# Kernel optimization log

Hardware: AMD Instinct MI355X
Metric: run time of the kernel (lower is better)

The kernel has to match this reference:

```python
import jax, jax.numpy as jnp
import numpy as np

B, S, D, H = 4, 2048, 1024, 16
DK = D // H

def setup_inputs() -> dict:
    key = jax.random.key(0)
    ks = jax.random.split(key, 11)
    s = 1.0 / np.sqrt(D)
    return {
        "query": jax.random.normal(ks[0], (B, S, D), jnp.float32),
        "key": jax.random.normal(ks[1], (B, S, D), jnp.float32),
        "value": jax.random.normal(ks[2], (B, S, D), jnp.float32),
        "Wq_w": jax.random.normal(ks[3], (D, D), jnp.float32) * s,
        "Wq_b": jnp.zeros((D,), jnp.float32),
        "Wk_w": jax.random.normal(ks[4], (D, D), jnp.float32) * s,
        "Wk_b": jnp.zeros((D,), jnp.float32),
        "Wv_w": jax.random.normal(ks[5], (D, D), jnp.float32) * s,
        "Wv_b": jnp.zeros((D,), jnp.float32),
        "Wo_w": jax.random.normal(ks[6], (D, D), jnp.float32) * s,
        "Wo_b": jnp.zeros((D,), jnp.float32),
    }

def reference(query, key, value, Wq_w, Wq_b, Wk_w, Wk_b, Wv_w, Wv_b, Wo_w, Wo_b):
    b, s, d = query.shape
    # Linear projections (torch Linear: x @ W.T + b)
    q = query @ Wq_w.T + Wq_b
    k = key @ Wk_w.T + Wk_b
    v = value @ Wv_w.T + Wv_b
    # split heads -> [B, H, S, DK]
    q = q.reshape(b, s, H, DK).transpose(0, 2, 1, 3)
    k = k.reshape(b, s, H, DK).transpose(0, 2, 1, 3)
    v = v.reshape(b, s, H, DK).transpose(0, 2, 1, 3)
    # scaled dot-product attention
    scores = jnp.einsum("bhqd,bhkd->bhqk", q, k) / jnp.sqrt(jnp.asarray(DK, q.dtype))
    attn = jax.nn.softmax(scores, axis=-1)
    z = jnp.einsum("bhqk,bhkd->bhqd", attn, v)
    # merge heads and output projection
    z = z.transpose(0, 2, 1, 3).reshape(b, s, H * DK)
    return z @ Wo_w.T + Wo_b
```

## Files before the change

kernel.cpp:

```cpp
#include <hip/hip_runtime.h>
#include <stdint.h>

typedef unsigned short u16;
typedef __bf16 bf16x8 __attribute__((ext_vector_type(8)));
typedef float f32x4 __attribute__((ext_vector_type(4)));

#define B_   4
#define S_   2048
#define D_   1024
#define H_   16
#define DK_  64
#define MTOK (B_*S_)
#define LOG2E 1.4426950408889634f

static __device__ __forceinline__ float exp2_fast(float x){
  return __builtin_amdgcn_exp2f(x);
}

static __device__ __forceinline__ void gload_lds16(const void* g, void* l){
  __builtin_amdgcn_global_load_lds(
      (const __attribute__((address_space(1))) unsigned int*)g,
      (__attribute__((address_space(3))) unsigned int*)l, 16, 0, 0);
}

union bf8pack { __bf16 h[8]; uint4 u; };

__global__ void cvt4(const float* __restrict__ s0, const float* __restrict__ s1,
                     const float* __restrict__ s2, const float* __restrict__ s3,
                     u16* __restrict__ out, int n8){
  const float* s = blockIdx.y==0 ? s0 : blockIdx.y==1 ? s1 : blockIdx.y==2 ? s2 : s3;
  u16* o = out + (size_t)blockIdx.y * ((size_t)n8 * 8);
  int i = blockIdx.x * blockDim.x + threadIdx.x;
  int stride = gridDim.x * blockDim.x;
  for (; i < n8; i += stride){
    float4 v0 = reinterpret_cast<const float4*>(s)[i*2];
    float4 v1 = reinterpret_cast<const float4*>(s)[i*2+1];
    bf8pack p;
    p.h[0]=(__bf16)v0.x; p.h[1]=(__bf16)v0.y; p.h[2]=(__bf16)v0.z; p.h[3]=(__bf16)v0.w;
    p.h[4]=(__bf16)v1.x; p.h[5]=(__bf16)v1.y; p.h[6]=(__bf16)v1.z; p.h[7]=(__bf16)v1.w;
    reinterpret_cast<uint4*>(o)[i] = p.u;
  }
}

__global__ __launch_bounds__(256) void gemm_qkv(
    const float* __restrict__ q_in, const float* __restrict__ k_in, const float* __restrict__ v_in,
    const u16* __restrict__ wq, const u16* __restrict__ wk, const u16* __restrict__ wv,
    const float* __restrict__ bq, const float* __restrict__ bk, const float* __restrict__ bv,
    u16* __restrict__ Qb, u16* __restrict__ Kb, u16* __restrict__ VtG){
  const int z = blockIdx.z;
  const float* Ap   = z==0 ? q_in : z==1 ? k_in : v_in;
  const u16*   Bw   = z==0 ? wq : z==1 ? wk : wv;
  const float* bias = z==0 ? bq : z==1 ? bk : bv;
  const float scale = z==0 ? 0.125f*LOG2E : 1.0f;
  u16* Cb = z==0 ? Qb : z==1 ? Kb : VtG;

  __shared__ u16 As[2][128][32];
  __shared__ u16 Bs[2][128][32];
  const int tid  = threadIdx.x;
  const int lane = tid & 63;
  const int wid  = tid >> 6;
  const int wr = wid >> 1, wc = wid & 1;
  const int r15 = lane & 15, q4 = lane >> 4;
  const int id = blockIdx.x;
  const int bm = (id & 7) + ((id >> 6) << 3);
  const int bn = (id >> 3) & 7;
  const int K = D_, N = D_;
  const int NT = K / 32;

  const int r = tid >> 2, c = (tid & 3) << 3;
  const float* Ar0 = Ap + (size_t)(bm*128 + r)*K + c;
  const float* Ar1 = Ap + (size_t)(bm*128 + r + 64)*K + c;
  const u16*  Br0 = Bw + (size_t)(bn*128 + r)*K + c;
  const u16*  Br1 = Bw + (size_t)(bn*128 + r + 64)*K + c;

  f32x4 acc[4][4] = {};

  {
    float4 v00 = *reinterpret_cast<const float4*>(Ar0);
    float4 v01 = *reinterpret_cast<const float4*>(Ar0 + 4);
    float4 v10 = *reinterpret_cast<const float4*>(Ar1);
    float4 v11 = *reinterpret_cast<const float4*>(Ar1 + 4);
    bf8pack p0, p1;
    p0.h[0]=(__bf16)v00.x; p0.h[1]=(__bf16)v00.y; p0.h[2]=(__bf16)v00.z; p0.h[3]=(__bf16)v00.w;
    p0.h[4]=(__bf16)v01.x; p0.h[5]=(__bf16)v01.y; p0.h[6]=(__bf16)v01.z; p0.h[7]=(__bf16)v01.w;
    p1.h[0]=(__bf16)v10.x; p1.h[1]=(__bf16)v10.y; p1.h[2]=(__bf16)v10.z; p1.h[3]=(__bf16)v10.w;
    p1.h[4]=(__bf16)v11.x; p1.h[5]=(__bf16)v11.y; p1.h[6]=(__bf16)v11.z; p1.h[7]=(__bf16)v11.w;
    *reinterpret_cast<uint4*>(&As[0][r][c])    = p0.u;
    *reinterpret_cast<uint4*>(&As[0][r+64][c]) = p1.u;
    gload_lds16(Br0, &Bs[0][r][c]);
    gload_lds16(Br1, &Bs[0][r+64][c]);
  }
  __syncthreads();

  for (int t = 0; t < NT; ++t){
    const int cur = t & 1;
    float4 v00, v01, v10, v11;
    const bool pf = (t + 1 < NT);
    if (pf){
      const float* p0 = Ar0 + (t+1)*32;
      const float* p1 = Ar1 + (t+1)*32;
      v00 = *reinterpret_cast<const float4*>(p0);
      v01 = *reinterpret_cast<const float4*>(p0 + 4);
      v10 = *reinterpret_cast<const float4*>(p1);
      v11 = *reinterpret_cast<const float4*>(p1 + 4);
      gload_lds16(Br0 + (t+1)*32, &Bs[cur^1][r][c]);
      gload_lds16(Br1 + (t+1)*32, &Bs[cur^1][r+64][c]);
    }

    bf16x8 af[4], bfr[4];
    #pragma unroll
    for (int mf = 0; mf < 4; ++mf)
      af[mf] = *reinterpret_cast<const bf16x8*>(&As[cur][wr*64 + mf*16 + r15][q4*8]);
    #pragma unroll
    for (int nf = 0; nf < 4; ++nf)
      bfr[nf] = *reinterpret_cast<const bf16x8*>(&Bs[cur][wc*64 + nf*16 + r15][q4*8]);
    #pragma unroll
    for (int mf = 0; mf < 4; ++mf)
      #pragma unroll
      for (int nf = 0; nf < 4; ++nf)
        acc[mf][nf] = __builtin_amdgcn_mfma_f32_16x16x32_bf16(af[mf], bfr[nf], acc[mf][nf], 0, 0, 0);

    if (pf){
      bf8pack p0, p1;
      p0.h[0]=(__bf16)v00.x; p0.h[1]=(__bf16)v00.y; p0.h[2]=(__bf16)v00.z; p0.h[3]=(__bf16)v00.w;
      p0.h[4]=(__bf16)v01.x; p0.h[5]=(__bf16)v01.y; p0.h[6]=(__bf16)v01.z; p0.h[7]=(__bf16)v01.w;
      p1.h[0]=(__bf16)v10.x; p1.h[1]=(__bf16)v10.y; p1.h[2]=(__bf16)v10.z; p1.h[3]=(__bf16)v10.w;
      p1.h[4]=(__bf16)v11.x; p1.h[5]=(__bf16)v11.y; p1.h[6]=(__bf16)v11.z; p1.h[7]=(__bf16)v11.w;
      *reinterpret_cast<uint4*>(&As[cur^1][r][c])    = p0.u;
      *reinterpret_cast<uint4*>(&As[cur^1][r+64][c]) = p1.u;
    }
    __syncthreads();
  }

  #pragma unroll
  for (int nf = 0; nf < 4; ++nf){
    int col = bn*128 + wc*64 + nf*16 + r15;
    float bv = bias[col];
    if (z == 2){
      int h = col >> 6, dk = col & 63;
      #pragma unroll
      for (int mf = 0; mf < 4; ++mf){
        int row0 = bm*128 + wr*64 + mf*16 + q4*4;
        int bb = row0 >> 11, s0 = row0 & (S_-1);
        bf8pack p;
        #pragma unroll
        for (int j = 0; j < 4; ++j) p.h[j] = (__bf16)(acc[mf][nf][j] + bv);
        uint2 u; u.x = p.u.x; u.y = p.u.y;
        *reinterpret_cast<uint2*>(&Cb[((size_t)(bb*H_ + h)*DK_ + dk)*S_ + s0]) = u;
      }
    } else {
      #pragma unroll
      for (int mf = 0; mf < 4; ++mf){
        #pragma unroll
        for (int j = 0; j < 4; ++j){
          int row = bm*128 + wr*64 + mf*16 + q4*4 + j;
          __bf16 hv = (__bf16)((acc[mf][nf][j] + bv) * scale);
          Cb[(size_t)row*N + col] = *reinterpret_cast<u16*>(&hv);
        }
      }
    }
  }
}

__global__ __launch_bounds__(256) void gemm_out(const u16* __restrict__ Ab,
    const u16* __restrict__ Bw, const float* __restrict__ bias, float* __restrict__ Cf){
  __shared__ u16 As[2][128][32];
  __shared__ u16 Bs[2][128][32];
  const int tid  = threadIdx.x;
  const int lane = tid & 63;
  const int wid  = tid >> 6;
  const int wr = wid >> 1, wc = wid & 1;
  const int r15 = lane & 15, q4 = lane >> 4;
  const int id = blockIdx.x;
  const int bm = (id & 7) + ((id >> 6) << 3);
  const int bn = (id >> 3) & 7;
  const int K = D_, N = D_;
  const int NT = K / 32;

  const int r = tid >> 2, c = (tid & 3) << 3;
  const u16* Ar0 = Ab + (size_t)(bm*128 + r)*K + c;
  const u16* Ar1 = Ab + (size_t)(bm*128 + r + 64)*K + c;
  const u16* Br0 = Bw + (size_t)(bn*128 + r)*K + c;
  const u16* Br1 = Bw + (size_t)(bn*128 + r + 64)*K + c;

  f32x4 acc[4][4] = {};

  gload_lds16(Ar0, &As[0][r][c]);
  gload_lds16(Ar1, &As[0][r+64][c]);
  gload_lds16(Br0, &Bs[0][r][c]);
  gload_lds16(Br1, &Bs[0][r+64][c]);
  __syncthreads();

  for (int t = 0; t < NT; ++t){
    const int cur = t & 1;
    if (t + 1 < NT){
      gload_lds16(Ar0 + (t+1)*32, &As[cur^1][r][c]);
      gload_lds16(Ar1 + (t+1)*32, &As[cur^1][r+64][c]);
      gload_lds16(Br0 + (t+1)*32, &Bs[cur^1][r][c]);
      gload_lds16(Br1 + (t+1)*32, &Bs[cur^1][r+64][c]);
    }

    bf16x8 af[4], bfr[4];
    #pragma unroll
    for (int mf = 0; mf < 4; ++mf)
      af[mf] = *reinterpret_cast<const bf16x8*>(&As[cur][wr*64 + mf*16 + r15][q4*8]);
    #pragma unroll
    for (int nf = 0; nf < 4; ++nf)
      bfr[nf] = *reinterpret_cast<const bf16x8*>(&Bs[cur][wc*64 + nf*16 + r15][q4*8]);
    #pragma unroll
    for (int mf = 0; mf < 4; ++mf)
      #pragma unroll
      for (int nf = 0; nf < 4; ++nf)
        acc[mf][nf] = __builtin_amdgcn_mfma_f32_16x16x32_bf16(af[mf], bfr[nf], acc[mf][nf], 0, 0, 0);
    __syncthreads();
  }

  #pragma unroll
  for (int nf = 0; nf < 4; ++nf){
    int col = bn*128 + wc*64 + nf*16 + r15;
    float bv = bias[col];
    #pragma unroll
    for (int mf = 0; mf < 4; ++mf)
      #pragma unroll
      for (int j = 0; j < 4; ++j){
        int row = bm*128 + wr*64 + mf*16 + q4*4 + j;
        Cf[(size_t)row*N + col] = acc[mf][nf][j] + bv;
      }
  }
}

__global__ __launch_bounds__(256) void attn128(const u16* __restrict__ Qg,
    const u16* __restrict__ Kg, const u16* __restrict__ VtG, u16* __restrict__ Zg){
  __shared__ u16 Ks[64][72];
  __shared__ u16 Vts[64][72];
  __shared__ __bf16 Ps[128][72];
  const int tid  = threadIdx.x;
  const int lane = tid & 63;
  const int wv   = tid >> 6;
  const int r15  = lane & 15, q4 = lane >> 4;
  const int qt = blockIdx.x;
  const int bh = blockIdx.y;
  const int b = bh >> 4, h = bh & (H_-1);
  const size_t baseQ = ((size_t)b * S_) * D_ + (size_t)h * DK_;
  const size_t baseV = (size_t)bh * DK_ * S_;
  const int q0 = qt * 128;

  bf16x8 aq[2][2];
  #pragma unroll
  for (int mf = 0; mf < 2; ++mf){
    const u16* qr = Qg + baseQ + (size_t)(q0 + wv*32 + mf*16 + r15) * D_;
    aq[mf][0] = *reinterpret_cast<const bf16x8*>(qr + q4*8);
    aq[mf][1] = *reinterpret_cast<const bf16x8*>(qr + 32 + q4*8);
  }

  bf16x8 vones;
  #pragma unroll
  for (int i = 0; i < 8; ++i) vones[i] = (__bf16)1.0f;

  const int srow = tid >> 3, scol = (tid & 7) << 3;
  const u16* Kbase = Kg + baseQ;
  const u16* Vbase = VtG + baseV;

  uint4 kreg0, kreg1, vreg0, vreg1;
  kreg0 = *reinterpret_cast<const uint4*>(Kbase + (size_t)srow*D_ + scol);
  kreg1 = *reinterpret_cast<const uint4*>(Kbase + (size_t)(srow+32)*D_ + scol);
  vreg0 = *reinterpret_cast<const uint4*>(Vbase + (size_t)srow*S_ + scol);
  vreg1 = *reinterpret_cast<const uint4*>(Vbase + (size_t)(srow+32)*S_ + scol);

  f32x4 o_acc[2][4] = {};
  f32x4 l_acc[2] = {};

  for (int kt = 0; kt < S_/64; ++kt){
    if (kt) __syncthreads();
    *reinterpret_cast<uint4*>(&Ks[srow][scol])      = kreg0;
    *reinterpret_cast<uint4*>(&Ks[srow+32][scol])   = kreg1;
    *reinterpret_cast<uint4*>(&Vts[srow][scol])     = vreg0;
    *reinterpret_cast<uint4*>(&Vts[srow+32][scol])  = vreg1;

    if (kt + 1 < S_/64){
      const u16* kp = Kbase + (size_t)((kt+1)*64 + srow)*D_ + scol;
      kreg0 = *reinterpret_cast<const uint4*>(kp);
      kreg1 = *reinterpret_cast<const uint4*>(kp + (size_t)32*D_);
      const u16* vp = Vbase + (size_t)srow*S_ + (kt+1)*64 + scol;
      vreg0 = *reinterpret_cast<const uint4*>(vp);
      vreg1 = *reinterpret_cast<const uint4*>(vp + (size_t)32*S_);
    }
    __syncthreads();

    bf16x8 bk[4][2];
    #pragma unroll
    for (int nf = 0; nf < 4; ++nf){
      bk[nf][0] = *reinterpret_cast<const bf16x8*>(&Ks[nf*16 + r15][q4*8]);
      bk[nf][1] = *reinterpret_cast<const bf16x8*>(&Ks[nf*16 + r15][32 + q4*8]);
    }

    #pragma unroll
    for (int mf = 0; mf < 2; ++mf){
      f32x4 sacc[4] = {};
      #pragma unroll
      for (int nf = 0; nf < 4; ++nf){
        sacc[nf] = __builtin_amdgcn_mfma_f32_16x16x32_bf16(aq[mf][0], bk[nf][0], sacc[nf], 0, 0, 0);
        sacc[nf] = __builtin_amdgcn_mfma_f32_16x16x32_bf16(aq[mf][1], bk[nf][1], sacc[nf], 0, 0, 0);
      }
      #pragma unroll
      for (int nf = 0; nf < 4; ++nf)
        #pragma unroll
        for (int j = 0; j < 4; ++j)
          Ps[wv*32 + mf*16 + q4*4 + j][nf*16 + r15] = (__bf16)exp2_fast(sacc[nf][j]);
    }

    #pragma unroll
    for (int ks = 0; ks < 2; ++ks){
      bf16x8 bvf[4];
      #pragma unroll
      for (int nf = 0; nf < 4; ++nf)
        bvf[nf] = *reinterpret_cast<const bf16x8*>(&Vts[nf*16 + r15][ks*32 + q4*8]);
      #pragma unroll
      for (int mf = 0; mf < 2; ++mf){
        uint2 plo = *reinterpret_cast<const uint2*>(&Ps[wv*32 + mf*16 + r15][ks*32 + q4*8]);
        uint2 phi = *reinterpret_cast<const uint2*>(&Ps[wv*32 + mf*16 + r15][ks*32 + q4*8 + 4]);
        uint4 pw; pw.x = plo.x; pw.y = plo.y; pw.z = phi.x; pw.w = phi.y;
        bf16x8 ap = *reinterpret_cast<bf16x8*>(&pw);
        #pragma unroll
        for (int nf = 0; nf < 4; ++nf)
          o_acc[mf][nf] = __builtin_amdgcn_mfma_f32_16x16x32_bf16(ap, bvf[nf], o_acc[mf][nf], 0, 0, 0);
        l_acc[mf] = __builtin_amdgcn_mfma_f32_16x16x32_bf16(ap, vones, l_acc[mf], 0, 0, 0);
      }
    }
  }

  #pragma unroll
  for (int mf = 0; mf < 2; ++mf){
    f32x4 inv;
    #pragma unroll
    for (int j = 0; j < 4; ++j) inv[j] = 1.0f / l_acc[mf][j];
    #pragma unroll
    for (int nf = 0; nf < 4; ++nf)
      #pragma unroll
      for (int j = 0; j < 4; ++j){
        int qrw = q0 + wv*32 + mf*16 + q4*4 + j;
        int col = nf*16 + r15;
        __bf16 hv = (__bf16)(o_acc[mf][nf][j] * inv[j]);
        Zg[baseQ + (size_t)qrw*D_ + col] = *reinterpret_cast<u16*>(&hv);
      }
  }
}

extern "C" void kernel_launch(void* const* d_in, const int* in_sizes, int n_in,
                              void* d_out, int out_size, void* d_ws, size_t ws_size,
                              hipStream_t stream){
  const float* q_in = (const float*)d_in[0];
  const float* k_in = (const float*)d_in[1];
  const float* v_in = (const float*)d_in[2];
  const float* Wq_w = (const float*)d_in[3];
  const float* Wq_b = (const float*)d_in[4];
  const float* Wk_w = (const float*)d_in[5];
  const float* Wk_b = (const float*)d_in[6];
  const float* Wv_w = (const float*)d_in[7];
  const float* Wv_b = (const float*)d_in[8];
  const float* Wo_w = (const float*)d_in[9];
  const float* Wo_b = (const float*)d_in[10];
  float* out = (float*)d_out;

  u16* ws = (u16*)d_ws;
  const size_t WE = (size_t)D_ * D_;
  const size_t XE = (size_t)MTOK * D_;
  u16* wqb = ws;
  u16* wkb = wqb + WE;
  u16* wvb = wkb + WE;
  u16* wob = wvb + WE;
  u16* Qb  = wob + WE;
  u16* Kb  = Qb + XE;
  u16* VtG = Kb + XE;
  u16* Zb  = VtG + XE;

  cvt4<<<dim3(128, 4), 256, 0, stream>>>(Wq_w, Wk_w, Wv_w, Wo_w, wqb, (int)(WE/8));

  dim3 gqkv((MTOK/128)*(D_/128), 1, 3), bb(256);
  gemm_qkv<<<gqkv, bb, 0, stream>>>(q_in, k_in, v_in, wqb, wkb, wvb,
                                    Wq_b, Wk_b, Wv_b, Qb, Kb, VtG);

  attn128<<<dim3(S_/128, B_*H_), bb, 0, stream>>>(Qb, Kb, VtG, Zb);

  gemm_out<<<dim3((MTOK/128)*(D_/128)), bb, 0, stream>>>(Zb, wob, Wo_b, out);
}
```

Baseline: 220.3 us.

## Enlarge QKV GEMM tile to 256x256 and double-buffer K/V in attention

The QKV projection GEMM moves from 128x128 tiles with 256 threads to 256x256 tiles with 512 threads. Each wave now computes a 128x64 sub-tile, which raises operand reuse from shared memory and cuts global traffic per output, but grid parallelism drops to 384 blocks and register pressure rises. The attention kernel gains double-buffered K and V tiles in shared memory, so the next tile is written while the current one is consumed. This removes one barrier per iteration at the cost of extra LDS.

```diff
diff --git a/kernel.cpp b/kernel.cpp
--- a/kernel.cpp
+++ b/kernel.cpp
@@ -42,7 +42,7 @@
   }
 }
 
-__global__ __launch_bounds__(256) void gemm_qkv(
+__global__ __launch_bounds__(512) void gemm_qkv(
     const float* __restrict__ q_in, const float* __restrict__ k_in, const float* __restrict__ v_in,
     const u16* __restrict__ wq, const u16* __restrict__ wk, const u16* __restrict__ wv,
     const float* __restrict__ bq, const float* __restrict__ bk, const float* __restrict__ bv,
@@ -54,26 +54,24 @@
   const float scale = z==0 ? 0.125f*LOG2E : 1.0f;
   u16* Cb = z==0 ? Qb : z==1 ? Kb : VtG;
 
-  __shared__ u16 As[2][128][32];
-  __shared__ u16 Bs[2][128][32];
+  __shared__ u16 As[2][256][32];
+  __shared__ u16 Bs[2][256][32];
   const int tid  = threadIdx.x;
   const int lane = tid & 63;
   const int wid  = tid >> 6;
-  const int wr = wid >> 1, wc = wid & 1;
+  const int wr = wid >> 2, wc = wid & 3;
   const int r15 = lane & 15, q4 = lane >> 4;
-  const int id = blockIdx.x;
-  const int bm = (id & 7) + ((id >> 6) << 3);
-  const int bn = (id >> 3) & 7;
+  const int bm = blockIdx.x, bn = blockIdx.y;
   const int K = D_, N = D_;
   const int NT = K / 32;
 
   const int r = tid >> 2, c = (tid & 3) << 3;
-  const float* Ar0 = Ap + (size_t)(bm*128 + r)*K + c;
-  const float* Ar1 = Ap + (size_t)(bm*128 + r + 64)*K + c;
-  const u16*  Br0 = Bw + (size_t)(bn*128 + r)*K + c;
-  const u16*  Br1 = Bw + (size_t)(bn*128 + r + 64)*K + c;
-
-  f32x4 acc[4][4] = {};
+  const float* Ar0 = Ap + (size_t)(bm*256 + r)*K + c;
+  const float* Ar1 = Ap + (size_t)(bm*256 + r + 128)*K + c;
+  const u16*  Br0 = Bw + (size_t)(bn*256 + r)*K + c;
+  const u16*  Br1 = Bw + (size_t)(bn*256 + r + 128)*K + c;
+
+  f32x4 acc[8][4] = {};
 
   {
     float4 v00 = *reinterpret_cast<const float4*>(Ar0);
@@ -85,10 +83,10 @@
     p0.h[4]=(__bf16)v01.x; p0.h[5]=(__bf16)v01.y; p0.h[6]=(__bf16)v01.z; p0.h[7]=(__bf16)v01.w;
     p1.h[0]=(__bf16)v10.x; p1.h[1]=(__bf16)v10.y; p1.h[2]=(__bf16)v10.z; p1.h[3]=(__bf16)v10.w;
     p1.h[4]=(__bf16)v11.x; p1.h[5]=(__bf16)v11.y; p1.h[6]=(__bf16)v11.z; p1.h[7]=(__bf16)v11.w;
-    *reinterpret_cast<uint4*>(&As[0][r][c])    = p0.u;
-    *reinterpret_cast<uint4*>(&As[0][r+64][c]) = p1.u;
+    *reinterpret_cast<uint4*>(&As[0][r][c])     = p0.u;
+    *reinterpret_cast<uint4*>(&As[0][r+128][c]) = p1.u;
     gload_lds16(Br0, &Bs[0][r][c]);
-    gload_lds16(Br1, &Bs[0][r+64][c]);
+    gload_lds16(Br1, &Bs[0][r+128][c]);
   }
   __syncthreads();
 
@@ -104,21 +102,20 @@
       v10 = *reinterpret_cast<const float4*>(p1);
       v11 = *reinterpret_cast<const float4*>(p1 + 4);
       gload_lds16(Br0 + (t+1)*32, &Bs[cur^1][r][c]);
-      gload_lds16(Br1 + (t+1)*32, &Bs[cur^1][r+64][c]);
-    }
-
-    bf16x8 af[4], bfr[4];
-    #pragma unroll
-    for (int mf = 0; mf < 4; ++mf)
-      af[mf] = *reinterpret_cast<const bf16x8*>(&As[cur][wr*64 + mf*16 + r15][q4*8]);
+      gload_lds16(Br1 + (t+1)*32, &Bs[cur^1][r+128][c]);
+    }
+
+    bf16x8 bfr[4];
     #pragma unroll
     for (int nf = 0; nf < 4; ++nf)
       bfr[nf] = *reinterpret_cast<const bf16x8*>(&Bs[cur][wc*64 + nf*16 + r15][q4*8]);
     #pragma unroll
-    for (int mf = 0; mf < 4; ++mf)
+    for (int mf = 0; mf < 8; ++mf){
+      bf16x8 af = *reinterpret_cast<const bf16x8*>(&As[cur][wr*128 + mf*16 + r15][q4*8]);
       #pragma unroll
       for (int nf = 0; nf < 4; ++nf)
-        acc[mf][nf] = __builtin_amdgcn_mfma_f32_16x16x32_bf16(af[mf], bfr[nf], acc[mf][nf], 0, 0, 0);
+        acc[mf][nf] = __builtin_amdgcn_mfma_f32_16x16x32_bf16(af, bfr[nf], acc[mf][nf], 0, 0, 0);
+    }
 
     if (pf){
       bf8pack p0, p1;
@@ -126,21 +123,21 @@
       p0.h[4]=(__bf16)v01.x; p0.h[5]=(__bf16)v01.y; p0.h[6]=(__bf16)v01.z; p0.h[7]=(__bf16)v01.w;
       p1.h[0]=(__bf16)v10.x; p1.h[1]=(__bf16)v10.y; p1.h[2]=(__bf16)v10.z; p1.h[3]=(__bf16)v10.w;
       p1.h[4]=(__bf16)v11.x; p1.h[5]=(__bf16)v11.y; p1.h[6]=(__bf16)v11.z; p1.h[7]=(__bf16)v11.w;
-      *reinterpret_cast<uint4*>(&As[cur^1][r][c])    = p0.u;
-      *reinterpret_cast<uint4*>(&As[cur^1][r+64][c]) = p1.u;
+      *reinterpret_cast<uint4*>(&As[cur^1][r][c])     = p0.u;
+      *reinterpret_cast<uint4*>(&As[cur^1][r+128][c]) = p1.u;
     }
     __syncthreads();
   }
 
   #pragma unroll
   for (int nf = 0; nf < 4; ++nf){
-    int col = bn*128 + wc*64 + nf*16 + r15;
+    int col = bn*256 + wc*64 + nf*16 + r15;
     float bv = bias[col];
     if (z == 2){
       int h = col >> 6, dk = col & 63;
       #pragma unroll
-      for (int mf = 0; mf < 4; ++mf){
-        int row0 = bm*128 + wr*64 + mf*16 + q4*4;
+      for (int mf = 0; mf < 8; ++mf){
+        int row0 = bm*256 + wr*128 + mf*16 + q4*4;
         int bb = row0 >> 11, s0 = row0 & (S_-1);
         bf8pack p;
         #pragma unroll
@@ -150,10 +147,10 @@
       }
     } else {
       #pragma unroll
-      for (int mf = 0; mf < 4; ++mf){
+      for (int mf = 0; mf < 8; ++mf){
         #pragma unroll
         for (int j = 0; j < 4; ++j){
-          int row = bm*128 + wr*64 + mf*16 + q4*4 + j;
+          int row = bm*256 + wr*128 + mf*16 + q4*4 + j;
           __bf16 hv = (__bf16)((acc[mf][nf][j] + bv) * scale);
           Cb[(size_t)row*N + col] = *reinterpret_cast<u16*>(&hv);
         }
@@ -231,8 +228,8 @@
 
 __global__ __launch_bounds__(256) void attn128(const u16* __restrict__ Qg,
     const u16* __restrict__ Kg, const u16* __restrict__ VtG, u16* __restrict__ Zg){
-  __shared__ u16 Ks[64][72];
-  __shared__ u16 Vts[64][72];
+  __shared__ u16 Ks[2][64][72];
+  __shared__ u16 Vts[2][64][72];
   __shared__ __bf16 Ps[128][72];
   const int tid  = threadIdx.x;
   const int lane = tid & 63;
@@ -270,28 +267,42 @@
   f32x4 o_acc[2][4] = {};
   f32x4 l_acc[2] = {};
 
+  *reinterpret_cast<uint4*>(&Ks[0][srow][scol])      = kreg0;
+  *reinterpret_cast<uint4*>(&Ks[0][srow+32][scol])   = kreg1;
+  *reinterpret_cast<uint4*>(&Vts[0][srow][scol])     = vreg0;
+  *reinterpret_cast<uint4*>(&Vts[0][srow+32][scol])  = vreg1;
+  {
+    const u16* kp = Kbase + (size_t)(64 + srow)*D_ + scol;
+    kreg0 = *reinterpret_cast<const uint4*>(kp);
+    kreg1 = *reinterpret_cast<const uint4*>(kp + (size_t)32*D_);
+    const u16* vp = Vbase + (size_t)srow*S_ + 64 + scol;
+    vreg0 = *reinterpret_cast<const uint4*>(vp);
+    vreg1 = *reinterpret_cast<const uint4*>(vp + (size_t)32*S_);
+  }
+  __syncthreads();
+
   for (int kt = 0; kt < S_/64; ++kt){
-    if (kt) __syncthreads();
-    *reinterpret_cast<uint4*>(&Ks[srow][scol])      = kreg0;
-    *reinterpret_cast<uint4*>(&Ks[srow+32][scol])   = kreg1;
-    *reinterpret_cast<uint4*>(&Vts[srow][scol])     = vreg0;
-    *reinterpret_cast<uint4*>(&Vts[srow+32][scol])  = vreg1;
-
+    const int cur = kt & 1;
     if (kt + 1 < S_/64){
-      const u16* kp = Kbase + (size_t)((kt+1)*64 + srow)*D_ + scol;
-      kreg0 = *reinterpret_cast<const uint4*>(kp);
-      kreg1 = *reinterpret_cast<const uint4*>(kp + (size_t)32*D_);
-      const u16* vp = Vbase + (size_t)srow*S_ + (kt+1)*64 + scol;
-      vreg0 = *reinterpret_cast<const uint4*>(vp);
-      vreg1 = *reinterpret_cast<const uint4*>(vp + (size_t)32*S_);
-    }
-    __syncthreads();
+      *reinterpret_cast<uint4*>(&Ks[cur^1][srow][scol])      = kreg0;
+      *reinterpret_cast<uint4*>(&Ks[cur^1][srow+32][scol])   = kreg1;
+      *reinterpret_cast<uint4*>(&Vts[cur^1][srow][scol])     = vreg0;
+      *reinterpret_cast<uint4*>(&Vts[cur^1][srow+32][scol])  = vreg1;
+      if (kt + 2 < S_/64){
+        const u16* kp = Kbase + (size_t)((kt+2)*64 + srow)*D_ + scol;
+        kreg0 = *reinterpret_cast<const uint4*>(kp);
+        kreg1 = *reinterpret_cast<const uint4*>(kp + (size_t)32*D_);
+        const u16* vp = Vbase + (size_t)srow*S_ + (kt+2)*64 + scol;
+        vreg0 = *reinterpret_cast<const uint4*>(vp);
+        vreg1 = *reinterpret_cast<const uint4*>(vp + (size_t)32*S_);
+      }
+    }
 
     bf16x8 bk[4][2];
     #pragma unroll
     for (int nf = 0; nf < 4; ++nf){
-      bk[nf][0] = *reinterpret_cast<const bf16x8*>(&Ks[nf*16 + r15][q4*8]);
-      bk[nf][1] = *reinterpret_cast<const bf16x8*>(&Ks[nf*16 + r15][32 + q4*8]);
+      bk[nf][0] = *reinterpret_cast<const bf16x8*>(&Ks[cur][nf*16 + r15][q4*8]);
+      bk[nf][1] = *reinterpret_cast<const bf16x8*>(&Ks[cur][nf*16 + r15][32 + q4*8]);
     }
 
     #pragma unroll
@@ -314,7 +325,7 @@
       bf16x8 bvf[4];
       #pragma unroll
       for (int nf = 0; nf < 4; ++nf)
-        bvf[nf] = *reinterpret_cast<const bf16x8*>(&Vts[nf*16 + r15][ks*32 + q4*8]);
+        bvf[nf] = *reinterpret_cast<const bf16x8*>(&Vts[cur][nf*16 + r15][ks*32 + q4*8]);
       #pragma unroll
       for (int mf = 0; mf < 2; ++mf){
         uint2 plo = *reinterpret_cast<const uint2*>(&Ps[wv*32 + mf*16 + r15][ks*32 + q4*8]);
@@ -327,6 +338,7 @@
         l_acc[mf] = __builtin_amdgcn_mfma_f32_16x16x32_bf16(ap, vones, l_acc[mf], 0, 0, 0);
       }
     }
+    __syncthreads();
   }
 
   #pragma unroll
@@ -376,11 +388,11 @@
 
   cvt4<<<dim3(128, 4), 256, 0, stream>>>(Wq_w, Wk_w, Wv_w, Wo_w, wqb, (int)(WE/8));
 
-  dim3 gqkv((MTOK/128)*(D_/128), 1, 3), bb(256);
-  gemm_qkv<<<gqkv, bb, 0, stream>>>(q_in, k_in, v_in, wqb, wkb, wvb,
+  dim3 gqkv(MTOK/256, D_/256, 3), bq(512);
+  gemm_qkv<<<gqkv, bq, 0, stream>>>(q_in, k_in, v_in, wqb, wkb, wvb,
                                     Wq_b, Wk_b, Wv_b, Qb, Kb, VtG);
 
-  attn128<<<dim3(S_/128, B_*H_), bb, 0, stream>>>(Qb, Kb, VtG, Zb);
-
-  gemm_out<<<dim3((MTOK/128)*(D_/128)), bb, 0, stream>>>(Zb, wob, Wo_b, out);
-}
+  attn128<<<dim3(S_/128, B_*H_), dim3(256), 0, stream>>>(Qb, Kb, VtG, Zb);
+
+  gemm_out<<<dim3((MTOK/128)*(D_/128)), dim3(256), 0, stream>>>(Zb, wob, Wo_b, out);
+}
```

Measured after the change: 255.1 us. +15.8%, slower.
